# Kernel tuning notes

Hardware: AMD Instinct MI355X
Metric: run time of the kernel (lower is better)

Reference implementation:

```python
import jax, jax.numpy as jnp
import numpy as np
import math

B, S, D = 2, 1024, 2048
NH, NKV, HD = 16, 8, 128
NREP = NH // NKV
WINDOW = 256  # = max_seq_len; ReRoPE window


def _rope(x, cos, sin):
    # x: (b, s, h, d); cos/sin broadcastable to (b, s, h, d//2). Interleaved pairs (llama2.c style).
    b, s, h, d = x.shape
    xr, xi = x[..., ::2], x[..., 1::2]
    or_ = xr * cos - xi * sin
    oi = xr * sin + xi * cos
    return jnp.stack([or_, oi], axis=-1).reshape(b, s, h, d)


def setup_inputs() -> dict:
    key = jax.random.key(0)
    kx, kq, kk, kv, ko = jax.random.split(key, 5)
    # real RoPE tables (theta=10000), per-position, half head dim
    inv = 1.0 / (10000.0 ** (np.arange(0, HD, 2, dtype=np.float32) / HD))
    fr = np.outer(np.arange(S, dtype=np.float32), inv).astype(np.float32)  # (S, HD//2)
    sc = 0.02
    return {
        "x": jax.random.normal(kx, (B, S, D), jnp.float32),
        "freqs_cos": jnp.asarray(np.cos(fr)),
        "freqs_sin": jnp.asarray(np.sin(fr)),
        "wq": jax.random.normal(kq, (D, NH * HD), jnp.float32) * sc,
        "wk": jax.random.normal(kk, (D, NKV * HD), jnp.float32) * sc,
        "wv": jax.random.normal(kv, (D, NKV * HD), jnp.float32) * sc,
        "wo": jax.random.normal(ko, (NH * HD, D), jnp.float32) * sc,
    }


def reference(x, freqs_cos, freqs_sin, wq, wk, wv, wo):
    b, s, _ = x.shape
    xq = (x @ wq).reshape(b, s, NH, HD)
    xk = (x @ wk).reshape(b, s, NKV, HD)
    xv = (x @ wv).reshape(b, s, NKV, HD)

    cos = freqs_cos[:s][None, :, None, :]
    sin = freqs_sin[:s][None, :, None, :]
    q1 = _rope(xq, cos, sin)   # standard RoPE
    k1 = _rope(xk, cos, sin)

    # ReRoPE: queries rotated at the fixed clamp position = window; keys unrotated
    cw = freqs_cos[WINDOW][None, None, None, :]
    sw = freqs_sin[WINDOW][None, None, None, :]
    q2 = _rope(xq, cw, sw)
    k2 = xk

    rep = lambda a: jnp.repeat(a, NREP, axis=2)          # repeat_kv (GQA)
    heads = lambda a: a.transpose(0, 2, 1, 3)            # (b, h, s, d)
    q1, k1, v = heads(q1), heads(rep(k1)), heads(rep(xv))
    q2, k2 = heads(q2), heads(rep(k2))

    scale = 1.0 / math.sqrt(HD)
    s1 = jnp.einsum("bhqd,bhkd->bhqk", q1, k1) * scale
    s2 = jnp.einsum("bhqd,bhkd->bhqk", q2, k2) * scale

    i = jnp.arange(s)[:, None]
    j = jnp.arange(s)[None, :]
    causal = j <= i
    rect = causal & (j > i - WINDOW)                     # rectified_mask band
    scores = jnp.where(rect, s1, s2)
    scores = jnp.where(causal, scores, -jnp.inf)         # mask_inf (causal)

    attn = jax.nn.softmax(scores.astype(jnp.float32), axis=-1).astype(x.dtype)
    out = jnp.einsum("bhqk,bhkd->bhqd", attn, v)
    out = out.transpose(0, 2, 1, 3).reshape(b, s, NH * HD)
    return out @ wo
```

## Files before the change

### kernel.cpp

```cpp
#include <hip/hip_runtime.h>
#include <hip/hip_bf16.h>

#define BDIM 2
#define SDIM 1024
#define DDIM 2048
#define NH 16
#define NKV 8
#define HD 128
#define WINDOW 256

typedef __bf16 bf16;
typedef __bf16 bf16x4 __attribute__((ext_vector_type(4)));
typedef __bf16 bf16x8 __attribute__((ext_vector_type(8)));
typedef float f32x4 __attribute__((ext_vector_type(4)));

#define L2E 1.44269504088896341f

__device__ inline bf16x8 load8(const bf16* p) { return *reinterpret_cast<const bf16x8*>(p); }

__device__ __forceinline__ void gl_lds16(const bf16* g, bf16* l) {
  __builtin_amdgcn_global_load_lds(
      (__attribute__((address_space(1))) void*)g,
      (__attribute__((address_space(3))) void*)l,
      16, 0, 0);
}

__global__ __launch_bounds__(256) void prep(const float* __restrict__ x,
                                            const float* __restrict__ wq,
                                            const float* __restrict__ wk,
                                            const float* __restrict__ wv,
                                            const float* __restrict__ wo,
                                            bf16* __restrict__ xb,
                                            bf16* __restrict__ wqkvT,
                                            bf16* __restrict__ woT) {
  __shared__ bf16 tile[32][33];
  int z = blockIdx.z;
  int tx = threadIdx.x, ty = threadIdx.y;
  if (z == 4) {
    long i = (((long)blockIdx.y * 64 + blockIdx.x) * 256 + ty * 32 + tx) * 4;
    float4 a = *(const float4*)(x + i);
    bf16x4 o;
    o[0] = (bf16)a.x; o[1] = (bf16)a.y; o[2] = (bf16)a.z; o[3] = (bf16)a.w;
    *(bf16x4*)(xb + i) = o;
    return;
  }
  const float* src; bf16* dst; int C;
  if (z == 0)      { src = wq; dst = wqkvT;                 C = 2048; }
  else if (z == 1) { src = wk; dst = wqkvT + 2048L * 2048;  C = 1024; }
  else if (z == 2) { src = wv; dst = wqkvT + 3072L * 2048;  C = 1024; }
  else             { src = wo; dst = woT;                   C = 2048; }
  int c0 = blockIdx.x * 32, r0 = blockIdx.y * 32;
  if (c0 >= C) return;
  for (int yy = ty; yy < 32; yy += 8)
    tile[yy][tx] = (bf16)src[(long)(r0 + yy) * C + c0 + tx];
  __syncthreads();
  for (int yy = ty; yy < 32; yy += 8)
    dst[(long)(c0 + yy) * 2048 + r0 + tx] = tile[tx][yy];
}

#define BK 64
__global__ __launch_bounds__(256) void gemm_bt_n64(const bf16* __restrict__ A,
                                                   const bf16* __restrict__ Bt,
                                                   float* __restrict__ C,
                                                   int M, int N, int K) {
  __shared__ bf16 smem[2 * 12288];
  int t = threadIdx.x;
  int wid = t >> 6, lane = t & 63;
  int wm = (wid >> 1) * 64, wn = (wid & 1) * 32;
  int fm = lane & 15, quad = lane >> 4;

  int wg = blockIdx.y * 32 + blockIdx.x;
  int swz = (wg & 7) * 64 + (wg >> 3);
  int by = swz >> 5, bx = swz & 31;
  int m0 = by * 128, n0 = bx * 64;

  const bf16* Ag = A + (long)m0 * K;
  const bf16* Bg = Bt + (long)n0 * K;

  f32x4 acc[4][2] = {};

  auto stA = [&](bf16* dst, int k0, int p) {
    int idx = p * 256 + t;
    int row = idx >> 3, ccs = idx & 7;
    int gcol = ((ccs ^ (row & 7)) * 8);
    gl_lds16(&Ag[(long)row * K + k0 + gcol], &dst[idx * 8]);
  };
  auto stB = [&](bf16* dst, int k0, int p) {
    int idx = p * 256 + t;
    int row = idx >> 3, ccs = idx & 7;
    int gcol = ((ccs ^ (row & 7)) * 8);
    gl_lds16(&Bg[(long)row * K + k0 + gcol], &dst[idx * 8]);
  };
  auto cmp = [&](const bf16* As, const bf16* Bs, int ks) {
    int cc = (ks >> 3) + quad;
    bf16x8 af[4], bfr[2];
    for (int i = 0; i < 4; ++i) {
      int fr = wm + i * 16 + fm;
      af[i] = load8(&As[(fr * 8 + (cc ^ (fr & 7))) * 8]);
    }
    for (int j = 0; j < 2; ++j) {
      int fr = wn + j * 16 + fm;
      bfr[j] = load8(&Bs[(fr * 8 + (cc ^ (fr & 7))) * 8]);
    }
    __builtin_amdgcn_s_setprio(1);
    for (int i = 0; i < 4; ++i)
      for (int j = 0; j < 2; ++j)
        acc[i][j] = __builtin_amdgcn_mfma_f32_16x16x32_bf16(af[i], bfr[j], acc[i][j], 0, 0, 0);
    __builtin_amdgcn_s_setprio(0);
  };

  {
    bf16* As = smem; bf16* Bs = smem + 8192;
    stA(As, 0, 0); stA(As, 0, 1); stA(As, 0, 2); stA(As, 0, 3);
    stB(Bs, 0, 0); stB(Bs, 0, 1);
  }
  const int NT = K / BK;
  for (int kt = 0; kt < NT; ++kt) {
    int cur = kt & 1;
    bf16* As = smem + cur * 12288;
    bf16* Bs = As + 8192;
    if (kt + 1 < NT) {
      bf16* An = smem + (cur ^ 1) * 12288;
      bf16* Bn = An + 8192;
      int kn = (kt + 1) * BK;
      stA(An, kn, 0); stA(An, kn, 1); stB(Bn, kn, 0);
      asm volatile("s_waitcnt vmcnt(3)\n\ts_barrier" ::: "memory");
      cmp(As, Bs, 0);
      stA(An, kn, 2); stA(An, kn, 3); stB(Bn, kn, 1);
      cmp(As, Bs, 32);
      asm volatile("s_barrier" ::: "memory");
    } else {
      asm volatile("s_waitcnt vmcnt(0)\n\ts_barrier" ::: "memory");
      cmp(As, Bs, 0);
      cmp(As, Bs, 32);
    }
  }
  for (int i = 0; i < 4; ++i)
    for (int r = 0; r < 4; ++r) {
      int row = m0 + wm + i * 16 + quad * 4 + r;
      for (int j = 0; j < 2; ++j) {
        int col = n0 + wn + j * 16 + fm;
        C[(long)row * N + col] = acc[i][j][r];
      }
    }
}

#define VPITCH 130
__global__ __launch_bounds__(512) void gemm_qkv(const bf16* __restrict__ A,
                                                const bf16* __restrict__ Bt,
                                                const float* __restrict__ fc,
                                                const float* __restrict__ fs,
                                                bf16* __restrict__ q0,
                                                bf16* __restrict__ k1,
                                                bf16* __restrict__ k2,
                                                bf16* __restrict__ vT) {
  const int K = 2048;
  __shared__ bf16 smem[2 * 24576];
  int t = threadIdx.x;
  int wid = t >> 6, lane = t & 63;
  int wm = (wid >> 2) * 64, wn = (wid & 3) * 64;
  int fm = lane & 15, quad = lane >> 4;

  int wg = blockIdx.y * 16 + blockIdx.x;
  int swz = (wg & 7) * 32 + (wg >> 3);
  int by = swz >> 4, bx = swz & 15;
  int m0 = by * 128, n0 = bx * 256;

  const bf16* Ag = A + (long)m0 * K;
  const bf16* Bg = Bt + (long)n0 * K;

  f32x4 acc[4][4] = {};

  auto stA = [&](bf16* dst, int k0, int p) {
    int idx = p * 512 + t;
    int row = idx >> 3, ccs = idx & 7;
    int gcol = ((ccs ^ (row & 7)) * 8);
    gl_lds16(&Ag[(long)row * K + k0 + gcol], &dst[idx * 8]);
  };
  auto stB = [&](bf16* dst, int k0, int p) {
    int idx = p * 512 + t;
    int row = idx >> 3, ccs = idx & 7;
    int gcol = ((ccs ^ (row & 7)) * 8);
    gl_lds16(&Bg[(long)row * K + k0 + gcol], &dst[idx * 8]);
  };
  auto cmp = [&](const bf16* As, const bf16* Bs, int ks) {
    int cc = (ks >> 3) + quad;
    bf16x8 af[4], bfr[4];
    for (int i = 0; i < 4; ++i) {
      int fr = wm + i * 16 + fm;
      af[i] = load8(&As[(fr * 8 + (cc ^ (fr & 7))) * 8]);
    }
    for (int j = 0; j < 4; ++j) {
      int fr = wn + j * 16 + fm;
      bfr[j] = load8(&Bs[(fr * 8 + (cc ^ (fr & 7))) * 8]);
    }
    __builtin_amdgcn_s_setprio(1);
    for (int i = 0; i < 4; ++i)
      for (int j = 0; j < 4; ++j)
        acc[i][j] = __builtin_amdgcn_mfma_f32_16x16x32_bf16(af[i], bfr[j], acc[i][j], 0, 0, 0);
    __builtin_amdgcn_s_setprio(0);
  };

  {
    bf16* As = smem; bf16* Bs = smem + 8192;
    stA(As, 0, 0); stA(As, 0, 1);
    stB(Bs, 0, 0); stB(Bs, 0, 1); stB(Bs, 0, 2); stB(Bs, 0, 3);
  }
  const int NT = K / 64;
  for (int kt = 0; kt < NT; ++kt) {
    int cur = kt & 1;
    bf16* As = smem + cur * 24576;
    bf16* Bs = As + 8192;
    if (kt + 1 < NT) {
      bf16* An = smem + (cur ^ 1) * 24576;
      bf16* Bn = An + 8192;
      int kn = (kt + 1) * 64;
      stA(An, kn, 0); stA(An, kn, 1); stB(Bn, kn, 0);
      asm volatile("s_waitcnt vmcnt(3)\n\ts_barrier" ::: "memory");
      cmp(As, Bs, 0);
      stB(Bn, kn, 1); stB(Bn, kn, 2); stB(Bn, kn, 3);
      cmp(As, Bs, 32);
      asm volatile("s_barrier" ::: "memory");
    } else {
      asm volatile("s_waitcnt vmcnt(0)\n\ts_barrier" ::: "memory");
      cmp(As, Bs, 0);
      cmp(As, Bs, 32);
    }
  }

  if (n0 < 2048) {
    const float scale = 0.08838834764831845f;
    for (int i = 0; i < 4; ++i)
      for (int r = 0; r < 4; ++r) {
        int row = m0 + wm + i * 16 + quad * 4 + r;
        for (int j = 0; j < 4; ++j) {
          int gc = n0 + wn + j * 16 + fm;
          q0[(long)row * 2048 + gc] = (bf16)(acc[i][j][r] * scale);
        }
      }
  } else if (n0 < 3072) {
    float sgn = (lane & 1) ? 1.f : -1.f;
    float cwj[4], swj[4];
    for (int j = 0; j < 4; ++j) {
      int dp = ((wn + j * 16 + fm) & 127) >> 1;
      cwj[j] = fc[WINDOW * 64 + dp];
      swj[j] = fs[WINDOW * 64 + dp] * (-sgn);
    }
    for (int i = 0; i < 4; ++i)
      for (int r = 0; r < 4; ++r) {
        int row = m0 + wm + i * 16 + quad * 4 + r;
        int s = row & (SDIM - 1);
        for (int j = 0; j < 4; ++j) {
          int kc = n0 - 2048 + wn + j * 16 + fm;
          int dp = (kc & 127) >> 1;
          float v = acc[i][j][r];
          float pp = __shfl_xor(v, 1, 64);
          float c = fc[s * 64 + dp];
          float sn = fs[s * 64 + dp] * sgn;
          long dst = (long)row * 1024 + kc;
          k1[dst] = (bf16)(v * c + pp * sn);
          k2[dst] = (bf16)(v * cwj[j] + pp * swj[j]);
        }
      }
  } else {
    int vv0 = (n0 - 3072) >> 7;
    int s0l = m0 & (SDIM - 1);
    int bq = m0 >> 10;
    for (int half = 0; half < 2; ++half) {
      __syncthreads();
      if (((wn >> 7) & 1) == half) {
        for (int i = 0; i < 4; ++i)
          for (int j = 0; j < 4; ++j) {
            int col = (wn & 127) + j * 16 + fm;
            for (int r = 0; r < 4; ++r) {
              int rl = wm + i * 16 + quad * 4 + r;
              smem[col * VPITCH + rl] = (bf16)acc[i][j][r];
            }
          }
      }
      __syncthreads();
      bf16* vtg = vT + ((long)(bq * NKV + vv0 + half)) * 128 * 1024;
      for (int p = 0; p < 4; ++p) {
        int c = p * 512 + t;
        int d = c >> 4, sc = (c & 15) * 8;
        *(bf16x8*)&vtg[(long)d * 1024 + s0l + sc] = *(bf16x8*)&smem[d * VPITCH + sc];
      }
    }
  }
}

__global__ __launch_bounds__(256) void attn_kernel(const bf16* __restrict__ q0,
                                                   const bf16* __restrict__ k1,
                                                   const bf16* __restrict__ k2,
                                                   const bf16* __restrict__ vT,
                                                   const float* __restrict__ fc,
                                                   const float* __restrict__ fs,
                                                   bf16* __restrict__ aout) {
  __shared__ bf16 Kb[2][8192];
  __shared__ bf16 Vb[2][8192];
  __shared__ bf16 Pl[4][16][72];
  __shared__ float stats[4][16];

  int h = blockIdx.y;
  int b = blockIdx.z;
  int tile = b ? (15 - blockIdx.x) : blockIdx.x;
  int kv = h >> 1;
  int t = threadIdx.x;
  int w = t >> 6, lane = t & 63;
  int m = lane & 15, quad = lane >> 4;

  const bf16* k1g0 = k1 + ((long)b * SDIM) * 1024 + kv * 128;
  const bf16* k2g0 = k2 + ((long)b * SDIM) * 1024 + kv * 128;
  const bf16* vtg0 = vT + ((long)(b * NKV + kv)) * 128 * 1024;

  int t0 = tile * 64;
  int i0w = t0 + w * 16;

  const bf16* q0p = q0 + ((long)(b * SDIM + i0w + m)) * 2048 + h * 128 + quad * 8;
  bf16x8 q0f[4], q1f[4];
  int srow = i0w + m;
  for (int kc = 0; kc < 4; ++kc) {
    q0f[kc] = load8(q0p + kc * 32);
    for (int p4 = 0; p4 < 4; ++p4) {
      int dp = kc * 16 + quad * 4 + p4;
      float c = fc[srow * 64 + dp], sn = fs[srow * 64 + dp];
      float xr = (float)q0f[kc][2 * p4], xi = (float)q0f[kc][2 * p4 + 1];
      q1f[kc][2 * p4]     = (bf16)(xr * c - xi * sn);
      q1f[kc][2 * p4 + 1] = (bf16)(xr * sn + xi * c);
    }
  }

  int NS2 = tile >= 4 ? tile - 3 : 0;
  int NSEG = NS2 + (tile < 4 ? tile + 1 : 5);
  int j1base = tile >= 4 ? t0 - 256 : 0;

  auto stage = [&](int s) {
    int j0, md;
    if (s < NS2) { j0 = s * 64; md = 2; } else { j0 = j1base + (s - NS2) * 64; md = 1; }
    const bf16* kg0 = (md == 1) ? k1g0 : k2g0;
    bf16* Kd = Kb[s & 1];
    bf16* Vd = Vb[s & 1];
    for (int p = 0; p < 4; ++p) {
      int idx = p * 256 + t;
      int kr = idx >> 4, kcs = idx & 15;
      int kg = (kcs ^ (kr & 15)) * 8;
      gl_lds16(&kg0[(long)(j0 + kr) * 1024 + kg], &Kd[idx * 8]);
      int vd = idx >> 3, vcs = idx & 7;
      int vg = (vcs ^ (vd & 7)) * 8;
      gl_lds16(&vtg0[(long)vd * 1024 + j0 + vg], &Vd[idx * 8]);
    }
  };

  f32x4 o[8] = {};
  float mrow = -INFINITY, lrow = 0.f;
  int i = i0w + m;

  stage(0);
  for (int s = 0; s < NSEG; ++s) {
    if (s + 1 < NSEG) {
      stage(s + 1);
      asm volatile("s_waitcnt vmcnt(8)\n\ts_barrier" ::: "memory");
    } else {
      asm volatile("s_waitcnt vmcnt(0)\n\ts_barrier" ::: "memory");
    }
    int j0, md;
    if (s < NS2) { j0 = s * 64; md = 2; } else { j0 = j1base + (s - NS2) * 64; md = 1; }
    bool fullseg = (md == 2) && (s < NS2 - 1);
    const bf16* Ks = Kb[s & 1];
    const bf16* VTs = Vb[s & 1];

    f32x4 sc[4] = {};
    if (md == 1) {
      for (int st = 0; st < 4; ++st)
        for (int kc = 0; kc < 4; ++kc) {
          int cc = kc * 4 + quad;
          sc[st] = __builtin_amdgcn_mfma_f32_16x16x32_bf16(
              load8(&Ks[((st * 16 + m) * 16 + (cc ^ m)) * 8]), q1f[kc], sc[st], 0, 0, 0);
        }
    } else {
      for (int st = 0; st < 4; ++st)
        for (int kc = 0; kc < 4; ++kc) {
          int cc = kc * 4 + quad;
          sc[st] = __builtin_amdgcn_mfma_f32_16x16x32_bf16(
              load8(&Ks[((st * 16 + m) * 16 + (cc ^ m)) * 8]), q0f[kc], sc[st], 0, 0, 0);
        }
    }

    float sv[4][4];
    for (int st = 0; st < 4; ++st)
      for (int r = 0; r < 4; ++r) {
        float v = sc[st][r];
        if (!fullseg) {
          int j = j0 + st * 16 + quad * 4 + r;
          if (md == 1) {
            if (j > i || j <= i - WINDOW) v = -INFINITY;
          } else {
            if (j > i - WINDOW) v = -INFINITY;
          }
        }
        sv[st][r] = v;
      }

    float bm = -INFINITY;
    for (int st = 0; st < 4; ++st)
      for (int r = 0; r < 4; ++r) bm = fmaxf(bm, sv[st][r]);
    bm = fmaxf(bm, __shfl_xor(bm, 16, 64));
    bm = fmaxf(bm, __shfl_xor(bm, 32, 64));
    float mnew = fmaxf(mrow, bm);
    float rs = 0.f;
    for (int st = 0; st < 4; ++st) {
      bf16x4 pk;
      for (int r = 0; r < 4; ++r) {
        float pvv = exp2f((sv[st][r] - mnew) * L2E);
        rs += pvv;
        pk[r] = (bf16)pvv;
      }
      *(bf16x4*)&Pl[w][m][st * 16 + quad * 4] = pk;
    }
    rs += __shfl_xor(rs, 16, 64);
    rs += __shfl_xor(rs, 32, 64);
    if (__any(mnew > mrow)) {
      float alpha = exp2f((mrow - mnew) * L2E);
      lrow = lrow * alpha + rs;
      mrow = mnew;
      if (lane < 16) stats[w][lane] = alpha;
      f32x4 av = *(f32x4*)&stats[w][quad * 4];
      for (int n8 = 0; n8 < 8; ++n8)
        for (int r = 0; r < 4; ++r) o[n8][r] *= av[r];
    } else {
      lrow += rs;
    }

    for (int kc = 0; kc < 2; ++kc) {
      bf16x8 af = load8(&Pl[w][m][kc * 32 + quad * 8]);
      int cc = kc * 4 + quad;
      for (int n8 = 0; n8 < 8; ++n8) {
        int d = n8 * 16 + m;
        o[n8] = __builtin_amdgcn_mfma_f32_16x16x32_bf16(
            af, load8(&VTs[(d * 8 + (cc ^ (d & 7))) * 8]), o[n8], 0, 0, 0);
      }
    }
    asm volatile("s_barrier" ::: "memory");
  }

  if (lane < 16) stats[w][lane] = lrow;
  __builtin_amdgcn_s_waitcnt(0);
  f32x4 lv = *(f32x4*)&stats[w][quad * 4];
  for (int n8 = 0; n8 < 8; ++n8)
    for (int r = 0; r < 4; ++r) {
      int row = i0w + quad * 4 + r;
      float val = o[n8][r] / lv[r];
      aout[((long)(b * SDIM + row)) * 2048 + h * 128 + n8 * 16 + m] = (bf16)val;
    }
}

extern "C" void kernel_launch(void* const* d_in, const int* in_sizes, int n_in,
                              void* d_out, int out_size, void* d_ws, size_t ws_size,
                              hipStream_t stream) {
  const float* x  = (const float*)d_in[0];
  const float* fc = (const float*)d_in[1];
  const float* fs = (const float*)d_in[2];
  const float* wq = (const float*)d_in[3];
  const float* wk = (const float*)d_in[4];
  const float* wv = (const float*)d_in[5];
  const float* wo = (const float*)d_in[6];
  float* out = (float*)d_out;

  bf16* wqkvT = (bf16*)d_ws;
  bf16* woT   = wqkvT + 4096L * 2048;
  bf16* xb    = woT + 2048L * 2048;
  bf16* q0b   = xb + 2048L * 2048;
  bf16* k1b   = q0b + 2048L * 2048;
  bf16* k2b   = k1b + 2048L * 1024;
  bf16* vT    = k2b + 2048L * 1024;
  bf16* aout  = vT + 2048L * 1024;

  prep<<<dim3(64, 64, 5), dim3(32, 8), 0, stream>>>(x, wq, wk, wv, wo, xb, wqkvT, woT);

  gemm_qkv<<<dim3(16, 16), 512, 0, stream>>>(xb, wqkvT, fc, fs, q0b, k1b, k2b, vT);

  attn_kernel<<<dim3(16, 16, 2), 256, 0, stream>>>(q0b, k1b, k2b, vT, fc, fs, aout);

  gemm_bt_n64<<<dim3(32, 16), 256, 0, stream>>>(aout, woT, out, 2048, 2048, 2048);
}
```

Before: 228.8 us.

## Triple-buffer K in LDS, load V directly to registers, lazy softmax rescale

The attention kernel now stages only K tiles through LDS, using a three-deep ring prefetched two segments ahead, and loads each segment's transposed V straight from global memory into registers. The online softmax starts from a fixed running max and only rescales the accumulators when a block max exceeds it by more than a threshold. s_setprio is raised around the MFMA sections. The aim is to cut LDS traffic and barrier stalls and to skip most rescale work. The cost is higher register pressure from the V fragments, and V global-load latency is now exposed inside each iteration.

```diff
diff --git a/kernel.cpp b/kernel.cpp
--- a/kernel.cpp
+++ b/kernel.cpp
@@ -296,8 +296,7 @@
                                                    const float* __restrict__ fc,
                                                    const float* __restrict__ fs,
                                                    bf16* __restrict__ aout) {
-  __shared__ bf16 Kb[2][8192];
-  __shared__ bf16 Vb[2][8192];
+  __shared__ bf16 Kb[3][8192];
   __shared__ bf16 Pl[4][16][72];
   __shared__ float stats[4][16];
 
@@ -315,15 +314,15 @@
 
   int t0 = tile * 64;
   int i0w = t0 + w * 16;
+  int i = i0w + m;
 
   const bf16* q0p = q0 + ((long)(b * SDIM + i0w + m)) * 2048 + h * 128 + quad * 8;
   bf16x8 q0f[4], q1f[4];
-  int srow = i0w + m;
   for (int kc = 0; kc < 4; ++kc) {
     q0f[kc] = load8(q0p + kc * 32);
     for (int p4 = 0; p4 < 4; ++p4) {
       int dp = kc * 16 + quad * 4 + p4;
-      float c = fc[srow * 64 + dp], sn = fs[srow * 64 + dp];
+      float c = fc[i * 64 + dp], sn = fs[i * 64 + dp];
       float xr = (float)q0f[kc][2 * p4], xi = (float)q0f[kc][2 * p4 + 1];
       q1f[kc][2 * p4]     = (bf16)(xr * c - xi * sn);
       q1f[kc][2 * p4 + 1] = (bf16)(xr * sn + xi * c);
@@ -334,42 +333,45 @@
   int NSEG = NS2 + (tile < 4 ? tile + 1 : 5);
   int j1base = tile >= 4 ? t0 - 256 : 0;
 
-  auto stage = [&](int s) {
-    int j0, md;
+  auto segj = [&](int s, int& j0, int& md) {
     if (s < NS2) { j0 = s * 64; md = 2; } else { j0 = j1base + (s - NS2) * 64; md = 1; }
+  };
+  auto stageK = [&](int s) {
+    int j0, md; segj(s, j0, md);
     const bf16* kg0 = (md == 1) ? k1g0 : k2g0;
-    bf16* Kd = Kb[s & 1];
-    bf16* Vd = Vb[s & 1];
+    bf16* Kd = Kb[s % 3];
     for (int p = 0; p < 4; ++p) {
       int idx = p * 256 + t;
       int kr = idx >> 4, kcs = idx & 15;
       int kg = (kcs ^ (kr & 15)) * 8;
       gl_lds16(&kg0[(long)(j0 + kr) * 1024 + kg], &Kd[idx * 8]);
-      int vd = idx >> 3, vcs = idx & 7;
-      int vg = (vcs ^ (vd & 7)) * 8;
-      gl_lds16(&vtg0[(long)vd * 1024 + j0 + vg], &Vd[idx * 8]);
     }
   };
 
   f32x4 o[8] = {};
-  float mrow = -INFINITY, lrow = 0.f;
-  int i = i0w + m;
-
-  stage(0);
+  float mrow = -30.f, lrow = 0.f;
+
+  stageK(0);
+  if (NSEG > 1) { stageK(1); asm volatile("s_waitcnt vmcnt(4)" ::: "memory"); }
+  else          {            asm volatile("s_waitcnt vmcnt(0)" ::: "memory"); }
+
   for (int s = 0; s < NSEG; ++s) {
-    if (s + 1 < NSEG) {
-      stage(s + 1);
-      asm volatile("s_waitcnt vmcnt(8)\n\ts_barrier" ::: "memory");
-    } else {
-      asm volatile("s_waitcnt vmcnt(0)\n\ts_barrier" ::: "memory");
-    }
-    int j0, md;
-    if (s < NS2) { j0 = s * 64; md = 2; } else { j0 = j1base + (s - NS2) * 64; md = 1; }
-    bool fullseg = (md == 2) && (s < NS2 - 1);
-    const bf16* Ks = Kb[s & 1];
-    const bf16* VTs = Vb[s & 1];
-
+    __builtin_amdgcn_s_barrier();
+    int j0, md; segj(s, j0, md);
+
+    bf16x8 vf0[8], vf1[8];
+#pragma unroll
+    for (int n8 = 0; n8 < 8; ++n8) {
+      long dbase = (long)(n8 * 16 + m) * 1024 + j0;
+      vf0[n8] = load8(&vtg0[dbase + quad * 8]);
+      vf1[n8] = load8(&vtg0[dbase + 32 + quad * 8]);
+    }
+    if (s + 2 < NSEG) stageK(s + 2);
+    __builtin_amdgcn_sched_barrier(0);
+
+    const bf16* Ks = Kb[s % 3];
     f32x4 sc[4] = {};
+    __builtin_amdgcn_s_setprio(1);
     if (md == 1) {
       for (int st = 0; st < 4; ++st)
         for (int kc = 0; kc < 4; ++kc) {
@@ -385,7 +387,9 @@
               load8(&Ks[((st * 16 + m) * 16 + (cc ^ m)) * 8]), q0f[kc], sc[st], 0, 0, 0);
         }
     }
-
+    __builtin_amdgcn_s_setprio(0);
+
+    bool fullseg = (md == 2) && (s < NS2 - 1);
     float sv[4][4];
     for (int st = 0; st < 4; ++st)
       for (int r = 0; r < 4; ++r) {
@@ -401,46 +405,52 @@
         sv[st][r] = v;
       }
 
+    float pv[4][4];
+    for (int st = 0; st < 4; ++st)
+      for (int r = 0; r < 4; ++r)
+        pv[st][r] = exp2f((sv[st][r] - mrow) * L2E);
     float bm = -INFINITY;
     for (int st = 0; st < 4; ++st)
       for (int r = 0; r < 4; ++r) bm = fmaxf(bm, sv[st][r]);
     bm = fmaxf(bm, __shfl_xor(bm, 16, 64));
     bm = fmaxf(bm, __shfl_xor(bm, 32, 64));
-    float mnew = fmaxf(mrow, bm);
+    if (!__all(bm <= mrow + 8.f)) {
+      float mnew = fmaxf(mrow, bm);
+      float alpha = exp2f((mrow - mnew) * L2E);
+      for (int st = 0; st < 4; ++st)
+        for (int r = 0; r < 4; ++r) pv[st][r] *= alpha;
+      lrow *= alpha;
+      if (lane < 16) stats[w][lane] = alpha;
+      f32x4 av = *(f32x4*)&stats[w][quad * 4];
+      for (int n8 = 0; n8 < 8; ++n8)
+        for (int r = 0; r < 4; ++r) o[n8][r] *= av[r];
+      mrow = mnew;
+    }
     float rs = 0.f;
     for (int st = 0; st < 4; ++st) {
       bf16x4 pk;
       for (int r = 0; r < 4; ++r) {
-        float pvv = exp2f((sv[st][r] - mnew) * L2E);
-        rs += pvv;
-        pk[r] = (bf16)pvv;
+        rs += pv[st][r];
+        pk[r] = (bf16)pv[st][r];
       }
       *(bf16x4*)&Pl[w][m][st * 16 + quad * 4] = pk;
     }
     rs += __shfl_xor(rs, 16, 64);
     rs += __shfl_xor(rs, 32, 64);
-    if (__any(mnew > mrow)) {
-      float alpha = exp2f((mrow - mnew) * L2E);
-      lrow = lrow * alpha + rs;
-      mrow = mnew;
-      if (lane < 16) stats[w][lane] = alpha;
-      f32x4 av = *(f32x4*)&stats[w][quad * 4];
+    lrow += rs;
+
+    {
+      bf16x8 af0 = load8(&Pl[w][m][quad * 8]);
+      bf16x8 af1 = load8(&Pl[w][m][32 + quad * 8]);
+      __builtin_amdgcn_s_setprio(1);
+#pragma unroll
       for (int n8 = 0; n8 < 8; ++n8)
-        for (int r = 0; r < 4; ++r) o[n8][r] *= av[r];
-    } else {
-      lrow += rs;
-    }
-
-    for (int kc = 0; kc < 2; ++kc) {
-      bf16x8 af = load8(&Pl[w][m][kc * 32 + quad * 8]);
-      int cc = kc * 4 + quad;
-      for (int n8 = 0; n8 < 8; ++n8) {
-        int d = n8 * 16 + m;
-        o[n8] = __builtin_amdgcn_mfma_f32_16x16x32_bf16(
-            af, load8(&VTs[(d * 8 + (cc ^ (d & 7))) * 8]), o[n8], 0, 0, 0);
-      }
-    }
-    asm volatile("s_barrier" ::: "memory");
+        o[n8] = __builtin_amdgcn_mfma_f32_16x16x32_bf16(af0, vf0[n8], o[n8], 0, 0, 0);
+#pragma unroll
+      for (int n8 = 0; n8 < 8; ++n8)
+        o[n8] = __builtin_amdgcn_mfma_f32_16x16x32_bf16(af1, vf1[n8], o[n8], 0, 0, 0);
+      __builtin_amdgcn_s_setprio(0);
+    }
   }
 
   if (lane < 16) stats[w][lane] = lrow;
```

Measured after the change: 233.4 us. +2.0%, slower.

## Share K/V tiles across GQA head pair and triple-buffer attention loads

Applied to the files above, without the earlier changes.

Each attention block now runs 8 waves and covers both query heads that share one KV head. Each K/V tile loaded into LDS is therefore reused by two heads, and the grid shrinks to half as many blocks. The LDS pipeline goes from double to triple buffering with a two-stage prefetch and adjusted vmcnt waits. s_setprio is raised around the MFMA loops. In exchange it uses more LDS per block and launches fewer, larger blocks, which may reduce how many blocks fit on each CU and how well the load is spread across CUs.

```diff
diff --git a/kernel.cpp b/kernel.cpp
--- a/kernel.cpp
+++ b/kernel.cpp
@@ -289,41 +289,42 @@
   }
 }
 
-__global__ __launch_bounds__(256) void attn_kernel(const bf16* __restrict__ q0,
+__global__ __launch_bounds__(512) void attn_kernel(const bf16* __restrict__ q0,
                                                    const bf16* __restrict__ k1,
                                                    const bf16* __restrict__ k2,
                                                    const bf16* __restrict__ vT,
                                                    const float* __restrict__ fc,
                                                    const float* __restrict__ fs,
                                                    bf16* __restrict__ aout) {
-  __shared__ bf16 Kb[2][8192];
-  __shared__ bf16 Vb[2][8192];
-  __shared__ bf16 Pl[4][16][72];
-  __shared__ float stats[4][16];
-
-  int h = blockIdx.y;
+  __shared__ bf16 Kb[3][8192];
+  __shared__ bf16 Vb[3][8192];
+  __shared__ bf16 Pl[8][16][72];
+  __shared__ float stats[8][16];
+
+  int kvh = blockIdx.y;
   int b = blockIdx.z;
   int tile = b ? (15 - blockIdx.x) : blockIdx.x;
-  int kv = h >> 1;
   int t = threadIdx.x;
   int w = t >> 6, lane = t & 63;
+  int wl = w & 3;
+  int h = kvh * 2 + (w >> 2);
   int m = lane & 15, quad = lane >> 4;
 
-  const bf16* k1g0 = k1 + ((long)b * SDIM) * 1024 + kv * 128;
-  const bf16* k2g0 = k2 + ((long)b * SDIM) * 1024 + kv * 128;
-  const bf16* vtg0 = vT + ((long)(b * NKV + kv)) * 128 * 1024;
+  const bf16* k1g0 = k1 + ((long)b * SDIM) * 1024 + kvh * 128;
+  const bf16* k2g0 = k2 + ((long)b * SDIM) * 1024 + kvh * 128;
+  const bf16* vtg0 = vT + ((long)(b * NKV + kvh)) * 128 * 1024;
 
   int t0 = tile * 64;
-  int i0w = t0 + w * 16;
+  int i0w = t0 + wl * 16;
+  int i = i0w + m;
 
   const bf16* q0p = q0 + ((long)(b * SDIM + i0w + m)) * 2048 + h * 128 + quad * 8;
   bf16x8 q0f[4], q1f[4];
-  int srow = i0w + m;
   for (int kc = 0; kc < 4; ++kc) {
     q0f[kc] = load8(q0p + kc * 32);
     for (int p4 = 0; p4 < 4; ++p4) {
       int dp = kc * 16 + quad * 4 + p4;
-      float c = fc[srow * 64 + dp], sn = fs[srow * 64 + dp];
+      float c = fc[i * 64 + dp], sn = fs[i * 64 + dp];
       float xr = (float)q0f[kc][2 * p4], xi = (float)q0f[kc][2 * p4 + 1];
       q1f[kc][2 * p4]     = (bf16)(xr * c - xi * sn);
       q1f[kc][2 * p4 + 1] = (bf16)(xr * sn + xi * c);
@@ -334,14 +335,16 @@
   int NSEG = NS2 + (tile < 4 ? tile + 1 : 5);
   int j1base = tile >= 4 ? t0 - 256 : 0;
 
+  auto segj = [&](int s, int& j0, int& md) {
+    if (s < NS2) { j0 = s * 64; md = 2; } else { j0 = j1base + (s - NS2) * 64; md = 1; }
+  };
   auto stage = [&](int s) {
-    int j0, md;
-    if (s < NS2) { j0 = s * 64; md = 2; } else { j0 = j1base + (s - NS2) * 64; md = 1; }
+    int j0, md; segj(s, j0, md);
     const bf16* kg0 = (md == 1) ? k1g0 : k2g0;
-    bf16* Kd = Kb[s & 1];
-    bf16* Vd = Vb[s & 1];
-    for (int p = 0; p < 4; ++p) {
-      int idx = p * 256 + t;
+    bf16* Kd = Kb[s % 3];
+    bf16* Vd = Vb[s % 3];
+    for (int p = 0; p < 2; ++p) {
+      int idx = p * 512 + t;
       int kr = idx >> 4, kcs = idx & 15;
       int kg = (kcs ^ (kr & 15)) * 8;
       gl_lds16(&kg0[(long)(j0 + kr) * 1024 + kg], &Kd[idx * 8]);
@@ -353,23 +356,27 @@
 
   f32x4 o[8] = {};
   float mrow = -INFINITY, lrow = 0.f;
-  int i = i0w + m;
 
   stage(0);
+  if (NSEG > 1) stage(1);
+
   for (int s = 0; s < NSEG; ++s) {
-    if (s + 1 < NSEG) {
-      stage(s + 1);
+    if (s + 2 < NSEG) {
+      stage(s + 2);
       asm volatile("s_waitcnt vmcnt(8)\n\ts_barrier" ::: "memory");
+    } else if (s + 1 < NSEG) {
+      asm volatile("s_waitcnt vmcnt(4)\n\ts_barrier" ::: "memory");
     } else {
       asm volatile("s_waitcnt vmcnt(0)\n\ts_barrier" ::: "memory");
     }
-    int j0, md;
-    if (s < NS2) { j0 = s * 64; md = 2; } else { j0 = j1base + (s - NS2) * 64; md = 1; }
+
+    int j0, md; segj(s, j0, md);
     bool fullseg = (md == 2) && (s < NS2 - 1);
-    const bf16* Ks = Kb[s & 1];
-    const bf16* VTs = Vb[s & 1];
+    const bf16* Ks = Kb[s % 3];
+    const bf16* VTs = Vb[s % 3];
 
     f32x4 sc[4] = {};
+    __builtin_amdgcn_s_setprio(1);
     if (md == 1) {
       for (int st = 0; st < 4; ++st)
         for (int kc = 0; kc < 4; ++kc) {
@@ -385,6 +392,7 @@
               load8(&Ks[((st * 16 + m) * 16 + (cc ^ m)) * 8]), q0f[kc], sc[st], 0, 0, 0);
         }
     }
+    __builtin_amdgcn_s_setprio(0);
 
     float sv[4][4];
     for (int st = 0; st < 4; ++st)
@@ -434,11 +442,13 @@
     for (int kc = 0; kc < 2; ++kc) {
       bf16x8 af = load8(&Pl[w][m][kc * 32 + quad * 8]);
       int cc = kc * 4 + quad;
+      __builtin_amdgcn_s_setprio(1);
       for (int n8 = 0; n8 < 8; ++n8) {
         int d = n8 * 16 + m;
         o[n8] = __builtin_amdgcn_mfma_f32_16x16x32_bf16(
             af, load8(&VTs[(d * 8 + (cc ^ (d & 7))) * 8]), o[n8], 0, 0, 0);
       }
+      __builtin_amdgcn_s_setprio(0);
     }
     asm volatile("s_barrier" ::: "memory");
   }
@@ -479,7 +489,7 @@
 
   gemm_qkv<<<dim3(16, 16), 512, 0, stream>>>(xb, wqkvT, fc, fs, q0b, k1b, k2b, vT);
 
-  attn_kernel<<<dim3(16, 16, 2), 256, 0, stream>>>(q0b, k1b, k2b, vT, fc, fs, aout);
+  attn_kernel<<<dim3(16, 8, 2), 512, 0, stream>>>(q0b, k1b, k2b, vT, fc, fs, aout);
 
   gemm_bt_n64<<<dim3(32, 16), 256, 0, stream>>>(aout, woT, out, 2048, 2048, 2048);
 }
```

New measurement: 229.1 us. Within noise of the previous version (+0.1%).
